# Kernel tuning notes

Measured on AMD Instinct MI355X. Metric: run time of the kernel, lower is better.

## Reference

```python
import jax, jax.numpy as jnp
import numpy as np

GEO_VOCAB = 32          # len(geo_code_char); class dim = GEO_VOCAB + 1 (padding idx)
A_VALUE = 0.8
SEQ = 12                # targets length, fixed by linspace(0,11,12) weight


def _integral(b, num_points=2000):
    # torch.linspace(0, b, 2000) includes endpoints; dx = b / num_points
    x = np.linspace(0.0, b, num_points)
    dx = b / num_points
    return np.sum(np.power(A_VALUE, x) * dx)

# continuous_rewards[0] = padding (0.0); rewards[i+1] = 1/integral(0, i+1)
CONT_REWARDS = np.array([0.0] + [1.0 / _integral(i + 1) for i in range(GEO_VOCAB)],
                        dtype=np.float32)
CORRECT_W = np.power(A_VALUE, np.arange(SEQ, dtype=np.float32)).astype(np.float32)
ERROR_W = (CORRECT_W + 1.0).astype(np.float32)


def _ce_none(logits, targets, ignore_index):
    # logits [B,S,V], targets [B,S]; per-element CE, 0 at ignored positions
    logp = jax.nn.log_softmax(logits, axis=-1)
    tgt = jnp.clip(targets, 0, logits.shape[-1] - 1)
    ce = -jnp.take_along_axis(logp, tgt[..., None], axis=-1)[..., 0]
    return jnp.where(targets == ignore_index, 0.0, ce)


def setup_inputs() -> dict:
    key = jax.random.key(0)
    k1, k2, k3, k4, k5, k6 = jax.random.split(key, 6)
    B, S, V = 131072, 13, GEO_VOCAB + 1
    return {
        "geo_output": jax.random.normal(k1, (B, S - 1, V), dtype=jnp.float32),
        "mask_geo_output": jax.random.normal(k2, (B, S, V), dtype=jnp.float32),
        "pos_geo_code": jax.random.randint(k3, (B, S), 0, V),
        "mask_ground_truth": jax.random.randint(k4, (B, S), 0, V),
        "aux_loss": jax.random.uniform(k5, (), dtype=jnp.float32),
        "token_aux_loss": jax.random.uniform(k6, (), dtype=jnp.float32),
        "sigma": jnp.ones((4,), dtype=jnp.float32),
    }


def reference(geo_output, mask_geo_output, pos_geo_code, mask_ground_truth,
              aux_loss, token_aux_loss, sigma):
    V = geo_output.shape[-1]
    ignore = V - 1  # len(geo_code_char)

    # mask loss: CE with ignore_index=-100, mean over valid positions
    logp_m = jax.nn.log_softmax(mask_geo_output, axis=-1)
    tgt_m = jnp.clip(mask_ground_truth, 0, V - 1)
    ce_m = -jnp.take_along_axis(logp_m, tgt_m[..., None], axis=-1)[..., 0]
    valid = (mask_ground_truth != -100).astype(ce_m.dtype)
    mask_loss = jnp.sum(ce_m * valid) / jnp.maximum(jnp.sum(valid), 1.0)

    # geo CE (reduction='none', ignore_index = V-1)
    targets = pos_geo_code[:, 1:]                       # [B, 12]
    cross_loss = _ce_none(geo_output, targets, ignore)  # [B, 12]

    correct = jnp.argmax(geo_output, axis=-1) == targets  # [B, 12] bool
    correct_mask = correct.astype(cross_loss.dtype)
    error_mask = 1.0 - correct_mask

    # first index where correct==False (argmin of int mask; 0 if all correct)
    min_idx = jnp.argmin(correct.astype(jnp.int32), axis=1)       # [B]
    prefix_mask = (jnp.arange(targets.shape[1]) < min_idx[:, None]).astype(cross_loss.dtype)
    cont = jnp.asarray(CONT_REWARDS)[min_idx][:, None]            # [B, 1]

    prefix_loss = jnp.mean(cross_loss * prefix_mask * cont)
    correct_loss = jnp.mean(cross_loss * correct_mask * jnp.asarray(CORRECT_W))
    error_loss = jnp.mean(cross_loss * error_mask * jnp.asarray(ERROR_W))
    geo_loss = prefix_loss + correct_loss + error_loss

    losses = jnp.stack([geo_loss, mask_loss, aux_loss, token_aux_loss])
    weighted = jnp.sum(0.5 * losses / sigma ** 2) + jnp.log(jnp.prod(sigma))

    return jnp.stack([weighted, prefix_loss, correct_loss, error_loss, mask_loss])
```

## Files before the change

### kernel.cpp

```cpp
#include <hip/hip_runtime.h>
#include <cmath>

#define THREADS 256
#define ROWS 16

struct Tables { float cont[12]; float cw[12]; float ew[12]; };

static Tables make_tables() {
    Tables tb;
    tb.cont[0] = 0.0f;
    for (int j = 1; j < 12; j++) {
        double b = (double)j;
        double s = 0.0;
        for (int k = 0; k < 2000; k++) {
            double x = b * (double)k / 1999.0;
            s += pow(0.8, x);
        }
        double integ = s * (b / 2000.0);
        tb.cont[j] = (float)(1.0 / integ);
    }
    for (int s = 0; s < 12; s++) {
        double w = pow(0.8, (double)s);
        tb.cw[s] = (float)w;
        tb.ew[s] = (float)(w + 1.0);
    }
    return tb;
}

__global__ void zero_acc(double* g) {
    if (threadIdx.x < 5) g[threadIdx.x] = 0.0;
}

__global__ __launch_bounds__(THREADS) void loss_main(
    const float* __restrict__ geo,
    const float* __restrict__ mgo,
    const int*   __restrict__ pos,
    const int*   __restrict__ mgt,
    double*      __restrict__ gacc,
    int B, Tables tb)
{
    __shared__ float buf[ROWS * 429];
    __shared__ int   s_pos[ROWS * 13];
    __shared__ int   s_mgt[ROWS * 13];
    __shared__ float s_ce[ROWS * 12];
    __shared__ int   s_corr[ROWS * 12];
    __shared__ float acc[5];

    const int t = threadIdx.x;
    const long long row0 = (long long)blockIdx.x * ROWS;
    const int nrows = min(ROWS, (int)(B - row0));
    if (nrows <= 0) return;

    if (t < 5) acc[t] = 0.0f;
    for (int i = t; i < nrows * 13; i += THREADS) {
        s_pos[i] = pos[row0 * 13 + i];
        s_mgt[i] = mgt[row0 * 13 + i];
    }
    {
        const float* src = mgo + row0 * 429;
        int nf = nrows * 429;
        int nf4 = nf >> 2;
        const float4* src4 = reinterpret_cast<const float4*>(src);
        float4* dst4 = reinterpret_cast<float4*>(buf);
        for (int i = t; i < nf4; i += THREADS) dst4[i] = src4[i];
        for (int i = (nf4 << 2) + t; i < nf; i += THREADS) buf[i] = src[i];
    }
    __syncthreads();

    if (t < nrows * 13) {
        const int r = t / 13, s = t - r * 13;
        const float* x = buf + r * 429 + s * 33;
        float m = x[0];
        #pragma unroll
        for (int k = 1; k < 33; k++) m = fmaxf(m, x[k]);
        float sum = 0.0f;
        #pragma unroll
        for (int k = 0; k < 33; k++) sum += expf(x[k] - m);
        float lse = logf(sum) + m;
        int tg = s_mgt[t];
        int tc = tg < 0 ? 0 : (tg > 32 ? 32 : tg);
        float ce = lse - x[tc];
        if (tg != -100) {
            atomicAdd(&acc[0], ce);
            atomicAdd(&acc[1], 1.0f);
        }
    }
    __syncthreads();

    {
        const float* src = geo + row0 * 396;
        int nf4 = (nrows * 396) >> 2;
        const float4* src4 = reinterpret_cast<const float4*>(src);
        float4* dst4 = reinterpret_cast<float4*>(buf);
        for (int i = t; i < nf4; i += THREADS) dst4[i] = src4[i];
    }
    __syncthreads();

    if (t < nrows * 12) {
        const int r = t / 12, s = t - r * 12;
        const float* x = buf + r * 396 + s * 33;
        float m = x[0]; int am = 0;
        #pragma unroll
        for (int k = 1; k < 33; k++) { float v = x[k]; if (v > m) { m = v; am = k; } }
        float sum = 0.0f;
        #pragma unroll
        for (int k = 0; k < 33; k++) sum += expf(x[k] - m);
        float lse = logf(sum) + m;
        int tg = s_pos[r * 13 + s + 1];
        int tc = tg < 0 ? 0 : (tg > 32 ? 32 : tg);
        float ce = (tg == 32) ? 0.0f : (lse - x[tc]);
        s_ce[t] = ce;
        s_corr[t] = (am == tg) ? 1 : 0;
    }
    __syncthreads();

    if (t < nrows) {
        int mi = 0;
        for (int s = 0; s < 12; s++) { if (!s_corr[t * 12 + s]) { mi = s; break; } }
        float cont = tb.cont[mi];
        float ps = 0.0f, cs = 0.0f, es = 0.0f;
        for (int s = 0; s < 12; s++) {
            float ce = s_ce[t * 12 + s];
            if (s < mi) ps += ce * cont;
            if (s_corr[t * 12 + s]) cs += ce * tb.cw[s];
            else                    es += ce * tb.ew[s];
        }
        atomicAdd(&acc[2], ps);
        atomicAdd(&acc[3], cs);
        atomicAdd(&acc[4], es);
    }
    __syncthreads();
    if (t < 5) atomicAdd(&gacc[t], (double)acc[t]);
}

__global__ void finalize(const double* __restrict__ g,
                         const float* __restrict__ aux,
                         const float* __restrict__ taux,
                         const float* __restrict__ sigma,
                         float* __restrict__ out, double denom)
{
    double mask_loss = g[0] / fmax(g[1], 1.0);
    double prefix = g[2] / denom;
    double corr   = g[3] / denom;
    double err    = g[4] / denom;
    double geo = prefix + corr + err;
    double L[4] = { geo, mask_loss, (double)aux[0], (double)taux[0] };
    double w = 0.0, prod = 1.0;
    for (int i = 0; i < 4; i++) {
        double sg = (double)sigma[i];
        w += 0.5 * L[i] / (sg * sg);
        prod *= sg;
    }
    w += log(prod);
    out[0] = (float)w;
    out[1] = (float)prefix;
    out[2] = (float)corr;
    out[3] = (float)err;
    out[4] = (float)mask_loss;
}

extern "C" void kernel_launch(void* const* d_in, const int* in_sizes, int n_in,
                              void* d_out, int out_size, void* d_ws, size_t ws_size,
                              hipStream_t stream)
{
    static Tables tb = make_tables();

    const float* geo   = (const float*)d_in[0];
    const float* mgo   = (const float*)d_in[1];
    const int*   pos   = (const int*)d_in[2];
    const int*   mgt   = (const int*)d_in[3];
    const float* aux   = (const float*)d_in[4];
    const float* taux  = (const float*)d_in[5];
    const float* sigma = (const float*)d_in[6];
    float* out = (float*)d_out;

    int B = in_sizes[2] / 13;
    double* gacc = (double*)d_ws;

    hipLaunchKernelGGL(zero_acc, dim3(1), dim3(64), 0, stream, gacc);
    int grid = (B + ROWS - 1) / ROWS;
    hipLaunchKernelGGL(loss_main, dim3(grid), dim3(THREADS), 0, stream,
                       geo, mgo, pos, mgt, gacc, B, tb);
    hipLaunchKernelGGL(finalize, dim3(1), dim3(1), 0, stream,
                       gacc, aux, taux, sigma, out, (double)B * 12.0);
}
```

Before: 481.2 us.

## Replace LDS-staged per-block kernel with thread-per-row direct loads and fused finalize

The shared-memory staging of 16 rows per block is replaced by one thread per geo row (12 positions handled serially) and one thread per mask position, each reading its 33 logits straight from global memory into registers. Reduction now uses wavefront shuffles plus a last-block counter that computes the final outputs, removing the separate finalize launch. It also switches to fast __expf/__logf. The risk is uncoalesced strided global loads: each thread reads a 1.5KB row, so a wavefront's accesses spread across many cache lines, and the float arrays use a lot of registers.

```diff
diff --git a/kernel.cpp b/kernel.cpp
--- a/kernel.cpp
+++ b/kernel.cpp
@@ -2,7 +2,6 @@
 #include <cmath>
 
 #define THREADS 256
-#define ROWS 16
 
 struct Tables { float cont[12]; float cw[12]; float ew[12]; };
 
@@ -28,135 +27,124 @@
 }
 
 __global__ void zero_acc(double* g) {
-    if (threadIdx.x < 5) g[threadIdx.x] = 0.0;
+    int t = threadIdx.x;
+    if (t < 5) g[t] = 0.0;
+    if (t == 5) *(unsigned int*)(g + 8) = 0u;
 }
 
-__global__ __launch_bounds__(THREADS) void loss_main(
+__global__ __launch_bounds__(THREADS) void loss_fused(
     const float* __restrict__ geo,
     const float* __restrict__ mgo,
     const int*   __restrict__ pos,
     const int*   __restrict__ mgt,
+    const float* __restrict__ aux,
+    const float* __restrict__ taux,
+    const float* __restrict__ sigma,
+    float*       __restrict__ out,
     double*      __restrict__ gacc,
-    int B, Tables tb)
+    unsigned int* __restrict__ counter,
+    int B, int geoBlocks, int totalBlocks, Tables tb)
 {
-    __shared__ float buf[ROWS * 429];
-    __shared__ int   s_pos[ROWS * 13];
-    __shared__ int   s_mgt[ROWS * 13];
-    __shared__ float s_ce[ROWS * 12];
-    __shared__ int   s_corr[ROWS * 12];
-    __shared__ float acc[5];
+    const int t = threadIdx.x;
+    float v0 = 0.0f, v1 = 0.0f, v2 = 0.0f;
+    const bool isGeo = (blockIdx.x < (unsigned)geoBlocks);
 
-    const int t = threadIdx.x;
-    const long long row0 = (long long)blockIdx.x * ROWS;
-    const int nrows = min(ROWS, (int)(B - row0));
-    if (nrows <= 0) return;
-
-    if (t < 5) acc[t] = 0.0f;
-    for (int i = t; i < nrows * 13; i += THREADS) {
-        s_pos[i] = pos[row0 * 13 + i];
-        s_mgt[i] = mgt[row0 * 13 + i];
-    }
-    {
-        const float* src = mgo + row0 * 429;
-        int nf = nrows * 429;
-        int nf4 = nf >> 2;
-        const float4* src4 = reinterpret_cast<const float4*>(src);
-        float4* dst4 = reinterpret_cast<float4*>(buf);
-        for (int i = t; i < nf4; i += THREADS) dst4[i] = src4[i];
-        for (int i = (nf4 << 2) + t; i < nf; i += THREADS) buf[i] = src[i];
-    }
-    __syncthreads();
-
-    if (t < nrows * 13) {
-        const int r = t / 13, s = t - r * 13;
-        const float* x = buf + r * 429 + s * 33;
-        float m = x[0];
-        #pragma unroll
-        for (int k = 1; k < 33; k++) m = fmaxf(m, x[k]);
-        float sum = 0.0f;
-        #pragma unroll
-        for (int k = 0; k < 33; k++) sum += expf(x[k] - m);
-        float lse = logf(sum) + m;
-        int tg = s_mgt[t];
-        int tc = tg < 0 ? 0 : (tg > 32 ? 32 : tg);
-        float ce = lse - x[tc];
-        if (tg != -100) {
-            atomicAdd(&acc[0], ce);
-            atomicAdd(&acc[1], 1.0f);
+    if (isGeo) {
+        int row = blockIdx.x * THREADS + t;
+        if (row < B) {
+            const float* xr = geo + (long long)row * 396;
+            const int*   pr = pos + (long long)row * 13 + 1;
+            float pssum = 0.0f, cs = 0.0f, es = 0.0f;
+            int mi = -1;
+            for (int s = 0; s < 12; s++) {
+                const float* xs = xr + s * 33;
+                float xv[33];
+                #pragma unroll
+                for (int k = 0; k < 33; k++) xv[k] = xs[k];
+                float m = xv[0]; int am = 0;
+                #pragma unroll
+                for (int k = 1; k < 33; k++) { if (xv[k] > m) { m = xv[k]; am = k; } }
+                float sum = 0.0f;
+                #pragma unroll
+                for (int k = 0; k < 33; k++) sum += __expf(xv[k] - m);
+                float lse = __logf(sum) + m;
+                int tg = pr[s];
+                int tc = tg < 0 ? 0 : (tg > 32 ? 32 : tg);
+                float ce = (tg == 32) ? 0.0f : (lse - xv[tc]);
+                bool corr = (am == tg);
+                if (corr) cs += ce * tb.cw[s]; else es += ce * tb.ew[s];
+                if (mi < 0) { if (corr) pssum += ce; else mi = s; }
+            }
+            if (mi < 0) { pssum = 0.0f; mi = 0; }
+            v0 = pssum * tb.cont[mi];
+            v1 = cs;
+            v2 = es;
+        }
+    } else {
+        long long task = (long long)(blockIdx.x - geoBlocks) * THREADS + t;
+        if (task < (long long)B * 13) {
+            int tg = mgt[task];
+            const float* xs = mgo + task * 33;
+            float xv[33];
+            #pragma unroll
+            for (int k = 0; k < 33; k++) xv[k] = xs[k];
+            float m = xv[0];
+            #pragma unroll
+            for (int k = 1; k < 33; k++) m = fmaxf(m, xv[k]);
+            float sum = 0.0f;
+            #pragma unroll
+            for (int k = 0; k < 33; k++) sum += __expf(xv[k] - m);
+            float lse = __logf(sum) + m;
+            int tc = tg < 0 ? 0 : (tg > 32 ? 32 : tg);
+            if (tg != -100) { v0 = lse - xv[tc]; v1 = 1.0f; }
         }
     }
+
+    #pragma unroll
+    for (int off = 32; off; off >>= 1) {
+        v0 += __shfl_down(v0, off, 64);
+        v1 += __shfl_down(v1, off, 64);
+        v2 += __shfl_down(v2, off, 64);
+    }
+    __shared__ float red[4][3];
+    const int wid = t >> 6, lane = t & 63;
+    if (lane == 0) { red[wid][0] = v0; red[wid][1] = v1; red[wid][2] = v2; }
     __syncthreads();
-
-    {
-        const float* src = geo + row0 * 396;
-        int nf4 = (nrows * 396) >> 2;
-        const float4* src4 = reinterpret_cast<const float4*>(src);
-        float4* dst4 = reinterpret_cast<float4*>(buf);
-        for (int i = t; i < nf4; i += THREADS) dst4[i] = src4[i];
+    if (t == 0) {
+        float a0 = 0, a1 = 0, a2 = 0;
+        for (int w = 0; w < 4; w++) { a0 += red[w][0]; a1 += red[w][1]; a2 += red[w][2]; }
+        if (isGeo) {
+            atomicAdd(&gacc[2], (double)a0);
+            atomicAdd(&gacc[3], (double)a1);
+            atomicAdd(&gacc[4], (double)a2);
+        } else {
+            atomicAdd(&gacc[0], (double)a0);
+            atomicAdd(&gacc[1], (double)a1);
+        }
+        __threadfence();
+        unsigned int old = atomicAdd(counter, 1u);
+        if (old == (unsigned)(totalBlocks - 1)) {
+            double g[5];
+            for (int i = 0; i < 5; i++) g[i] = atomicAdd(&gacc[i], 0.0);
+            double denom = (double)B * 12.0;
+            double mask_loss = g[0] / fmax(g[1], 1.0);
+            double prefix = g[2] / denom, corrL = g[3] / denom, errL = g[4] / denom;
+            double geoL = prefix + corrL + errL;
+            double L[4] = { geoL, mask_loss, (double)aux[0], (double)taux[0] };
+            double wsum = 0.0, prod = 1.0;
+            for (int i = 0; i < 4; i++) {
+                double sg = (double)sigma[i];
+                wsum += 0.5 * L[i] / (sg * sg);
+                prod *= sg;
+            }
+            wsum += log(prod);
+            out[0] = (float)wsum;
+            out[1] = (float)prefix;
+            out[2] = (float)corrL;
+            out[3] = (float)errL;
+            out[4] = (float)mask_loss;
+        }
     }
-    __syncthreads();
-
-    if (t < nrows * 12) {
-        const int r = t / 12, s = t - r * 12;
-        const float* x = buf + r * 396 + s * 33;
-        float m = x[0]; int am = 0;
-        #pragma unroll
-        for (int k = 1; k < 33; k++) { float v = x[k]; if (v > m) { m = v; am = k; } }
-        float sum = 0.0f;
-        #pragma unroll
-        for (int k = 0; k < 33; k++) sum += expf(x[k] - m);
-        float lse = logf(sum) + m;
-        int tg = s_pos[r * 13 + s + 1];
-        int tc = tg < 0 ? 0 : (tg > 32 ? 32 : tg);
-        float ce = (tg == 32) ? 0.0f : (lse - x[tc]);
-        s_ce[t] = ce;
-        s_corr[t] = (am == tg) ? 1 : 0;
-    }
-    __syncthreads();
-
-    if (t < nrows) {
-        int mi = 0;
-        for (int s = 0; s < 12; s++) { if (!s_corr[t * 12 + s]) { mi = s; break; } }
-        float cont = tb.cont[mi];
-        float ps = 0.0f, cs = 0.0f, es = 0.0f;
-        for (int s = 0; s < 12; s++) {
-            float ce = s_ce[t * 12 + s];
-            if (s < mi) ps += ce * cont;
-            if (s_corr[t * 12 + s]) cs += ce * tb.cw[s];
-            else                    es += ce * tb.ew[s];
-        }
-        atomicAdd(&acc[2], ps);
-        atomicAdd(&acc[3], cs);
-        atomicAdd(&acc[4], es);
-    }
-    __syncthreads();
-    if (t < 5) atomicAdd(&gacc[t], (double)acc[t]);
-}
-
-__global__ void finalize(const double* __restrict__ g,
-                         const float* __restrict__ aux,
-                         const float* __restrict__ taux,
-                         const float* __restrict__ sigma,
-                         float* __restrict__ out, double denom)
-{
-    double mask_loss = g[0] / fmax(g[1], 1.0);
-    double prefix = g[2] / denom;
-    double corr   = g[3] / denom;
-    double err    = g[4] / denom;
-    double geo = prefix + corr + err;
-    double L[4] = { geo, mask_loss, (double)aux[0], (double)taux[0] };
-    double w = 0.0, prod = 1.0;
-    for (int i = 0; i < 4; i++) {
-        double sg = (double)sigma[i];
-        w += 0.5 * L[i] / (sg * sg);
-        prod *= sg;
-    }
-    w += log(prod);
-    out[0] = (float)w;
-    out[1] = (float)prefix;
-    out[2] = (float)corr;
-    out[3] = (float)err;
-    out[4] = (float)mask_loss;
 }
 
 extern "C" void kernel_launch(void* const* d_in, const int* in_sizes, int n_in,
@@ -176,11 +164,15 @@
 
     int B = in_sizes[2] / 13;
     double* gacc = (double*)d_ws;
+    unsigned int* counter = (unsigned int*)((char*)d_ws + 64);
+
+    int geoBlocks  = (B + THREADS - 1) / THREADS;
+    long long maskTasks = (long long)B * 13;
+    int maskBlocks = (int)((maskTasks + THREADS - 1) / THREADS);
+    int totalBlocks = geoBlocks + maskBlocks;
 
     hipLaunchKernelGGL(zero_acc, dim3(1), dim3(64), 0, stream, gacc);
-    int grid = (B + ROWS - 1) / ROWS;
-    hipLaunchKernelGGL(loss_main, dim3(grid), dim3(THREADS), 0, stream,
-                       geo, mgo, pos, mgt, gacc, B, tb);
-    hipLaunchKernelGGL(finalize, dim3(1), dim3(1), 0, stream,
-                       gacc, aux, taux, sigma, out, (double)B * 12.0);
+    hipLaunchKernelGGL(loss_fused, dim3(totalBlocks), dim3(THREADS), 0, stream,
+                       geo, mgo, pos, mgt, aux, taux, sigma, out,
+                       gacc, counter, B, geoBlocks, totalBlocks, tb);
 }
```

After: 921.7 us. +91.5%, slower.
